# Performance work log

Hardware: AMD Instinct MI355X
Metric: run time of the kernel (lower is better)

Reference implementation:

```python
import math
import jax, jax.numpy as jnp
import numpy as np

D_MODEL = 1024
N_HEADS = 16
D_K = D_MODEL // N_HEADS
ROPE_BASE = 10000.0


def _rope_cos_sin(T, d, dtype=jnp.float32):
    inv_freq = 1.0 / (ROPE_BASE ** (jnp.arange(0, d, 2, dtype=jnp.float32) / d))
    ang = jnp.arange(T, dtype=jnp.float32)[:, None] * inv_freq[None, :]  # (T, d/2)
    emb = jnp.concatenate([ang, ang], axis=-1)  # (T, d)
    return jnp.cos(emb).astype(dtype), jnp.sin(emb).astype(dtype)


def _rotate_half(x):
    half = x.shape[-1] // 2
    return jnp.concatenate([-x[..., half:], x[..., :half]], axis=-1)


def _apply_rope(q, k):
    # q,k: (B, H, T, d_k)
    T = q.shape[2]
    cos, sin = _rope_cos_sin(T, q.shape[-1], q.dtype)  # (T, d_k)
    cos = cos[None, None]
    sin = sin[None, None]
    q = q * cos + _rotate_half(q) * sin
    k = k * cos + _rotate_half(k) * sin
    return q, k


def setup_inputs() -> dict:
    key = jax.random.key(0)
    ks = jax.random.split(key, 9)
    B, T = 4, 2048
    std = 1.0 / math.sqrt(D_MODEL)
    inp = {
        "x": jax.random.normal(ks[0], (B, T, D_MODEL), dtype=jnp.float32),
        "mask": jnp.zeros((B, 1, 1, T), dtype=bool),
        "Wq": jax.random.normal(ks[1], (D_MODEL, D_MODEL), jnp.float32) * std,
        "bq": jnp.zeros((D_MODEL,), jnp.float32),
        "Wk": jax.random.normal(ks[2], (D_MODEL, D_MODEL), jnp.float32) * std,
        "bk": jnp.zeros((D_MODEL,), jnp.float32),
        "Wv": jax.random.normal(ks[3], (D_MODEL, D_MODEL), jnp.float32) * std,
        "bv": jnp.zeros((D_MODEL,), jnp.float32),
        "Wo": jax.random.normal(ks[4], (D_MODEL, D_MODEL), jnp.float32) * std,
        "bo": jnp.zeros((D_MODEL,), jnp.float32),
    }
    return inp


def reference(x, mask, Wq, bq, Wk, bk, Wv, bv, Wo, bo):
    B, T, _ = x.shape
    H, dk = N_HEADS, D_K

    def proj(W, b):
        y = jnp.einsum("btd,ed->bte", x, W) + b  # nn.Linear: x @ W.T + b
        return y.reshape(B, T, H, dk).transpose(0, 2, 1, 3)  # (B,H,T,dk)

    q = proj(Wq, bq)
    k = proj(Wk, bk)
    v = proj(Wv, bv)
    q, k = _apply_rope(q, k)

    scale = math.sqrt(dk)
    scores = jnp.einsum("bhqd,bhkd->bhqk", q, k) / scale  # (B,H,T,T)
    neg = jnp.asarray(jnp.finfo(scores.dtype).min, scores.dtype)
    scores = jnp.where(mask, neg, scores)
    attn = jax.nn.softmax(scores, axis=-1)
    out = jnp.einsum("bhqk,bhkd->bhqd", attn, v)  # (B,H,T,dk)
    out = out.transpose(0, 2, 1, 3).reshape(B, T, H * dk)
    return jnp.einsum("btd,ed->bte", out, Wo) + bo
```

## Files before the change

### kernel.cpp

```cpp
#include <hip/hip_runtime.h>
#include <cstdint>

#define TSEQ   2048
#define NHEAD  16
#define DMODEL 1024
#define BSZ    4
#define MTOK   (BSZ*TSEQ)

typedef float  f32x4  __attribute__((ext_vector_type(4)));
typedef float  f32x16 __attribute__((ext_vector_type(16)));
typedef __bf16 bf16x8 __attribute__((ext_vector_type(8)));
typedef __bf16 bf16x4 __attribute__((ext_vector_type(4)));

static __device__ __forceinline__ f32x4 mfma16(bf16x8 a, bf16x8 b, f32x4 c) {
  return __builtin_amdgcn_mfma_f32_16x16x32_bf16(a, b, c, 0, 0, 0);
}
static __device__ __forceinline__ f32x16 mfma32(bf16x8 a, bf16x8 b, f32x16 c) {
  return __builtin_amdgcn_mfma_f32_32x32x16_bf16(a, b, c, 0, 0, 0);
}

#if __has_builtin(__builtin_amdgcn_exp2f)
#define EXP2(x) __builtin_amdgcn_exp2f(x)
#else
#define EXP2(x) exp2f(x)
#endif

static __device__ __forceinline__ uint32_t pk2(float lo, float hi) {
  union { __bf16 h[2]; uint32_t u; } cv;
  cv.h[0] = (__bf16)lo; cv.h[1] = (__bf16)hi;
  return cv.u;
}

static __device__ __forceinline__ void lds_cp16(void* lds, const void* g) {
  __builtin_amdgcn_global_load_lds(
      (__attribute__((address_space(1))) unsigned int*)(uintptr_t)g,
      (__attribute__((address_space(3))) unsigned int*)lds,
      16, 0, 0);
}


__global__ __launch_bounds__(256) void prep_cvt(
    const float* __restrict__ x,  const float* __restrict__ wq,
    const float* __restrict__ wk, const float* __restrict__ wv,
    const float* __restrict__ wo,
    __bf16* __restrict__ xb,  __bf16* __restrict__ wqb,
    __bf16* __restrict__ wkb, __bf16* __restrict__ wvb,
    __bf16* __restrict__ wob,
    float* __restrict__ ct, float* __restrict__ st)
{
  const int blk = blockIdx.x;
  if (blk >= 6144) {
    int i = (blk - 6144) * 256 + threadIdx.x;
    int t = i >> 5, d = i & 31;
    float inv = exp2f(-0.41524101186091903f * (float)d);
    float a = (float)t * inv;
    ct[i] = __cosf(a);
    st[i] = __sinf(a);
    return;
  }
  size_t i = (size_t)blk * 256 + threadIdx.x;
  const float* src; __bf16* dst; size_t base;
  if (i < 1048576) { src = x; dst = xb; base = i * 8; }
  else {
    size_t j = i - 1048576;
    int w = (int)(j >> 17);
    base = (j & 131071) * 8;
    switch (w) {
      case 0:  src = wq; dst = wqb; break;
      case 1:  src = wk; dst = wkb; break;
      case 2:  src = wv; dst = wvb; break;
      default: src = wo; dst = wob; break;
    }
  }
  float4 a = *reinterpret_cast<const float4*>(src + base);
  float4 b = *reinterpret_cast<const float4*>(src + base + 4);
  bf16x8 o;
  o[0] = (__bf16)a.x; o[1] = (__bf16)a.y; o[2] = (__bf16)a.z; o[3] = (__bf16)a.w;
  o[4] = (__bf16)b.x; o[5] = (__bf16)b.y; o[6] = (__bf16)b.z; o[7] = (__bf16)b.w;
  *reinterpret_cast<bf16x8*>(dst + base) = o;
}

__global__ __launch_bounds__(256) void gemm_qkv(
    const __bf16* __restrict__ A,
    const __bf16* __restrict__ Wqb, const __bf16* __restrict__ Wkb,
    const __bf16* __restrict__ Wvb,
    const float* __restrict__ bqp, const float* __restrict__ bkp,
    const float* __restrict__ bvp,
    __bf16* __restrict__ Qf, __bf16* __restrict__ Kf, __bf16* __restrict__ Vf,
    const float* __restrict__ ct, const float* __restrict__ st)
{
  __shared__ __align__(16) __bf16 As[128 * 32];
  __shared__ __align__(16) __bf16 Bs[128 * 32];

  const int bx = blockIdx.x;
  const int region = bx >> 3;
  const int n0 = (bx & 7) * 128;
  const __bf16* W = region == 0 ? Wqb : region == 1 ? Wkb : Wvb;
  const float* bias = region == 0 ? bqp : region == 1 ? bkp : bvp;
  const float qscale = region == 0 ? 0.18033688011112042f : 1.0f;

  const int tid  = threadIdx.x;
  const int wid  = tid >> 6, lane = tid & 63;
  const int wr   = wid >> 1, wc = wid & 1;
  const int lr   = lane & 15, lg = lane >> 4;
  const int m0   = blockIdx.y * 128;

  const int c0   = wid * 2;
  const int srow = lane >> 2;
  const int scol = (lane & 3) * 8;
  const __bf16* gA0 = A + (size_t)(m0 + c0 * 16 + srow) * 1024 + scol;
  const __bf16* gA1 = A + (size_t)(m0 + c0 * 16 + 16 + srow) * 1024 + scol;
  const __bf16* gB0 = W + (size_t)(n0 + c0 * 16 + srow) * 1024 + scol;
  const __bf16* gB1 = W + (size_t)(n0 + c0 * 16 + 16 + srow) * 1024 + scol;
  __bf16* lA0 = As + c0 * 512 + lane * 8;
  __bf16* lA1 = As + (c0 + 1) * 512 + lane * 8;
  __bf16* lB0 = Bs + c0 * 512 + lane * 8;
  __bf16* lB1 = Bs + (c0 + 1) * 512 + lane * 8;

  f32x4 acc[4][4] = {};

  for (int kt = 0; kt < 32; ++kt) {
    const int k0 = kt * 32;
    __syncthreads();
    lds_cp16(lA0, gA0 + k0);
    lds_cp16(lA1, gA1 + k0);
    lds_cp16(lB0, gB0 + k0);
    lds_cp16(lB1, gB1 + k0);
    __syncthreads();

    bf16x8 af[4], bf[4];
#pragma unroll
    for (int mi = 0; mi < 4; ++mi)
      af[mi] = *reinterpret_cast<const bf16x8*>(As + (wr * 64 + mi * 16 + lr) * 32 + lg * 8);
#pragma unroll
    for (int nj = 0; nj < 4; ++nj)
      bf[nj] = *reinterpret_cast<const bf16x8*>(Bs + (wc * 64 + nj * 16 + lr) * 32 + lg * 8);
#pragma unroll
    for (int mi = 0; mi < 4; ++mi)
#pragma unroll
      for (int nj = 0; nj < 4; ++nj)
        acc[mi][nj] = mfma16(af[mi], bf[nj], acc[mi][nj]);
  }

  float bcol[4];
#pragma unroll
  for (int nj = 0; nj < 4; ++nj) bcol[nj] = bias[n0 + wc * 64 + nj * 16 + lr];

  if (region < 2) {
    __bf16* Of = region == 0 ? Qf : Kf;
#pragma unroll
    for (int mi = 0; mi < 4; ++mi) {
      const int mbase = m0 + wr * 64 + mi * 16 + lg * 4;
#pragma unroll
      for (int r = 0; r < 4; ++r) {
        const int m = mbase + r;
        const int t = m & (TSEQ - 1);
        float v[4];
#pragma unroll
        for (int nj = 0; nj < 4; ++nj) v[nj] = acc[mi][nj][r] + bcol[nj];
#pragma unroll
        for (int nj = 0; nj < 4; ++nj) {
          const int idx = ((nj & 1) << 4) + lr;
          const float c = ct[t * 32 + idx];
          const float s = st[t * 32 + idx];
          const float rot = (nj < 2) ? -v[nj + 2] : v[nj - 2];
          const float o = (v[nj] * c + rot * s) * qscale;
          const int n = n0 + wc * 64 + nj * 16 + lr;
          const int d = n & 63, h = n >> 6;
          const int bh = ((m >> 11) << 4) + h;
          const size_t fidx =
              ((((size_t)bh * 64 + (t >> 5)) * 4 + (d >> 4)) * 2 + ((d >> 3) & 1)) * 256
              + (t & 31) * 8 + (d & 7);
          Of[fidx] = (__bf16)o;
        }
      }
    }
  } else {
#pragma unroll
    for (int mi = 0; mi < 4; ++mi) {
      const int mbase = m0 + wr * 64 + mi * 16 + lg * 4;
      const int bidx = mbase >> 11;
      const int tbase = mbase & (TSEQ - 1);
#pragma unroll
      for (int nj = 0; nj < 4; ++nj) {
        const int n = n0 + wc * 64 + nj * 16 + lr;
        const int h = n >> 6, d = n & 63;
        const int bh = bidx * 16 + h;
        bf16x4 pk;
#pragma unroll
        for (int r = 0; r < 4; ++r) pk[r] = (__bf16)(acc[mi][nj][r] + bcol[nj]);
        const size_t fidx =
            (((((size_t)bh * 32 + (tbase >> 6)) * 4 + ((tbase >> 4) & 3)) * 2
              + ((tbase >> 3) & 1)) * 2 + (d >> 5)) * 256
            + (d & 31) * 8 + (tbase & 7);
        *reinterpret_cast<bf16x4*>(Vf + fidx) = pk;
      }
    }
  }
}

__global__ __launch_bounds__(256) void gemm_out(
    const __bf16* __restrict__ A, const __bf16* __restrict__ W,
    const float* __restrict__ bias, float* __restrict__ Of)
{
  __shared__ __align__(16) __bf16 As[128 * 32];
  __shared__ __align__(16) __bf16 Bs[128 * 32];

  const int tid  = threadIdx.x;
  const int wid  = tid >> 6, lane = tid & 63;
  const int wr   = wid >> 1, wc = wid & 1;
  const int lr   = lane & 15, lg = lane >> 4;
  const int n0   = blockIdx.x * 128;
  const int m0   = blockIdx.y * 128;

  const int c0   = wid * 2;
  const int srow = lane >> 2;
  const int scol = (lane & 3) * 8;
  const __bf16* gA0 = A + (size_t)(m0 + c0 * 16 + srow) * 1024 + scol;
  const __bf16* gA1 = A + (size_t)(m0 + c0 * 16 + 16 + srow) * 1024 + scol;
  const __bf16* gB0 = W + (size_t)(n0 + c0 * 16 + srow) * 1024 + scol;
  const __bf16* gB1 = W + (size_t)(n0 + c0 * 16 + 16 + srow) * 1024 + scol;
  __bf16* lA0 = As + c0 * 512 + lane * 8;
  __bf16* lA1 = As + (c0 + 1) * 512 + lane * 8;
  __bf16* lB0 = Bs + c0 * 512 + lane * 8;
  __bf16* lB1 = Bs + (c0 + 1) * 512 + lane * 8;

  f32x4 acc[4][4] = {};

  for (int kt = 0; kt < 32; ++kt) {
    const int k0 = kt * 32;
    __syncthreads();
    lds_cp16(lA0, gA0 + k0);
    lds_cp16(lA1, gA1 + k0);
    lds_cp16(lB0, gB0 + k0);
    lds_cp16(lB1, gB1 + k0);
    __syncthreads();

    bf16x8 af[4], bf[4];
#pragma unroll
    for (int mi = 0; mi < 4; ++mi)
      af[mi] = *reinterpret_cast<const bf16x8*>(As + (wr * 64 + mi * 16 + lr) * 32 + lg * 8);
#pragma unroll
    for (int nj = 0; nj < 4; ++nj)
      bf[nj] = *reinterpret_cast<const bf16x8*>(Bs + (wc * 64 + nj * 16 + lr) * 32 + lg * 8);
#pragma unroll
    for (int mi = 0; mi < 4; ++mi)
#pragma unroll
      for (int nj = 0; nj < 4; ++nj)
        acc[mi][nj] = mfma16(af[mi], bf[nj], acc[mi][nj]);
  }

  float bcol[4];
#pragma unroll
  for (int nj = 0; nj < 4; ++nj) bcol[nj] = bias[n0 + wc * 64 + nj * 16 + lr];

#pragma unroll
  for (int mi = 0; mi < 4; ++mi) {
    const int mbase = m0 + wr * 64 + mi * 16 + lg * 4;
#pragma unroll
    for (int r = 0; r < 4; ++r) {
      const int m = mbase + r;
#pragma unroll
      for (int nj = 0; nj < 4; ++nj) {
        const int n = n0 + wc * 64 + nj * 16 + lr;
        Of[(size_t)m * 1024 + n] = acc[mi][nj][r] + bcol[nj];
      }
    }
  }
}

__global__ __launch_bounds__(128, 3) void attn_k(
    const __bf16* __restrict__ QKq, const __bf16* __restrict__ QKk,
    const __bf16* __restrict__ Vf, __bf16* __restrict__ O)
{
  const int tid = threadIdx.x, wid = tid >> 6, lane = tid & 63;
  const int ql = lane & 31, hl = lane >> 5;
  const int bid = blockIdx.x;
  const int bh = (bid & 7) * 8 + (bid >> 8);
  const int qt = (bid >> 3) & 31;
  const int b = bh >> 4, h = bh & 15;
  const int qbase = qt * 64 + wid * 32;
  const size_t tokQ = (size_t)b * TSEQ + qbase;
  const int laneoff = hl * 256 + ql * 8;

  const __bf16* Qb = QKq + ((size_t)bh * 64 + (qbase >> 5)) * 2048;
  bf16x8 qf[4];
#pragma unroll
  for (int ch = 0; ch < 4; ++ch)
    qf[ch] = *reinterpret_cast<const bf16x8*>(Qb + ch * 512 + laneoff);

  bf16x8 ones8;
#pragma unroll
  for (int j = 0; j < 8; ++j) ones8[j] = (__bf16)1.0f;

  f32x16 ot[2] = {};
  f32x16 lsum = {};

  const __bf16* Kbh = QKk + (size_t)bh * 64 * 2048;
  const __bf16* Vbh = Vf + (size_t)bh * 32 * 4096;

  for (int kv = 0; kv < TSEQ; kv += 64) {
    const __bf16* Vb = Vbh + (size_t)(kv >> 6) * 4096;
    bf16x8 va[2][4];
#pragma unroll
    for (int db = 0; db < 2; ++db)
#pragma unroll
      for (int c = 0; c < 4; ++c)
        va[db][c] = *reinterpret_cast<const bf16x8*>(
            Vb + c * 1024 + hl * 512 + db * 256 + ql * 8);

    bf16x8 ka[2][4];
#pragma unroll
    for (int s = 0; s < 2; ++s) {
      const __bf16* Kb = Kbh + (size_t)((kv >> 5) + s) * 2048;
#pragma unroll
      for (int ch = 0; ch < 4; ++ch)
        ka[s][ch] = *reinterpret_cast<const bf16x8*>(Kb + ch * 512 + laneoff);
    }

    f32x16 sx[2] = {};
    __builtin_amdgcn_s_setprio(1);
#pragma unroll
    for (int s = 0; s < 2; ++s)
#pragma unroll
      for (int ch = 0; ch < 4; ++ch)
        sx[s] = mfma32(ka[s][ch], qf[ch], sx[s]);
    __builtin_amdgcn_s_setprio(0);

    uint32_t pd[2][4][2];
#pragma unroll
    for (int s = 0; s < 2; ++s)
#pragma unroll
      for (int g = 0; g < 4; ++g)
#pragma unroll
        for (int hf = 0; hf < 2; ++hf)
          pd[s][g][hf] = pk2(EXP2(sx[s][4 * g + 2 * hf]),
                             EXP2(sx[s][4 * g + 2 * hf + 1]));

    uint32_t kp[2][2][2], rv[2][2][2];
#pragma unroll
    for (int s = 0; s < 2; ++s)
#pragma unroll
      for (int cc = 0; cc < 2; ++cc)
#pragma unroll
        for (int hf = 0; hf < 2; ++hf) {
          const uint32_t sendv = hl ? pd[s][2 * cc][hf] : pd[s][2 * cc + 1][hf];
          rv[s][cc][hf] = __shfl_xor(sendv, 32, 64);
          kp[s][cc][hf] = hl ? pd[s][2 * cc + 1][hf] : pd[s][2 * cc][hf];
        }

#pragma unroll
    for (int c = 0; c < 4; ++c) {
      const int s = c >> 1, cc = c & 1;
      union { uint32_t u[4]; bf16x8 v; } fb;
      fb.u[0] = hl ? rv[s][cc][0] : kp[s][cc][0];
      fb.u[1] = hl ? rv[s][cc][1] : kp[s][cc][1];
      fb.u[2] = hl ? kp[s][cc][0] : rv[s][cc][0];
      fb.u[3] = hl ? kp[s][cc][1] : rv[s][cc][1];
      __builtin_amdgcn_s_setprio(1);
      ot[0] = mfma32(va[0][c], fb.v, ot[0]);
      ot[1] = mfma32(va[1][c], fb.v, ot[1]);
      lsum  = mfma32(ones8,    fb.v, lsum);
      __builtin_amdgcn_s_setprio(0);
    }
  }

  const float inv = 1.0f / lsum[0];
  __bf16* Orow = O + (tokQ + ql) * 1024 + h * 64;
#pragma unroll
  for (int db = 0; db < 2; ++db)
#pragma unroll
    for (int g = 0; g < 4; ++g) {
      bf16x4 ov;
#pragma unroll
      for (int r = 0; r < 4; ++r) ov[r] = (__bf16)(ot[db][4 * g + r] * inv);
      *reinterpret_cast<bf16x4*>(Orow + db * 32 + 8 * g + 4 * hl) = ov;
    }
}

extern "C" void kernel_launch(void* const* d_in, const int* in_sizes, int n_in,
                              void* d_out, int out_size, void* d_ws, size_t ws_size,
                              hipStream_t stream) {
  (void)in_sizes; (void)n_in; (void)out_size; (void)ws_size;
  const float* x  = (const float*)d_in[0];
  const float* Wq = (const float*)d_in[2];
  const float* bq = (const float*)d_in[3];
  const float* Wk = (const float*)d_in[4];
  const float* bk = (const float*)d_in[5];
  const float* Wv = (const float*)d_in[6];
  const float* bvp= (const float*)d_in[7];
  const float* Wo = (const float*)d_in[8];
  const float* bo = (const float*)d_in[9];
  float* out = (float*)d_out;

  char* ws = (char*)d_ws;
  size_t off = 0;
  auto carve = [&](size_t bytes) { void* p = ws + off; off += (bytes + 255) & ~(size_t)255; return p; };
  __bf16* xb  = (__bf16*)carve((size_t)MTOK * DMODEL * 2);
  __bf16* qb  = (__bf16*)carve((size_t)MTOK * DMODEL * 2);
  __bf16* kb_ = (__bf16*)carve((size_t)MTOK * DMODEL * 2);
  __bf16* vt  = (__bf16*)carve((size_t)MTOK * DMODEL * 2);
  __bf16* ab  = (__bf16*)carve((size_t)MTOK * DMODEL * 2);
  __bf16* wqb = (__bf16*)carve((size_t)DMODEL * DMODEL * 2);
  __bf16* wkb = (__bf16*)carve((size_t)DMODEL * DMODEL * 2);
  __bf16* wvb = (__bf16*)carve((size_t)DMODEL * DMODEL * 2);
  __bf16* wob = (__bf16*)carve((size_t)DMODEL * DMODEL * 2);
  float*  ct  = (float*)carve((size_t)TSEQ * 32 * 4);
  float*  st  = (float*)carve((size_t)TSEQ * 32 * 4);

  prep_cvt<<<6400, 256, 0, stream>>>(x, Wq, Wk, Wv, Wo, xb, wqb, wkb, wvb, wob, ct, st);

  gemm_qkv<<<dim3(24, 64), 256, 0, stream>>>(xb, wqb, wkb, wvb, bq, bk, bvp,
                                             qb, kb_, vt, ct, st);

  attn_k<<<2048, 128, 0, stream>>>(qb, kb_, vt, ab);

  gemm_out<<<dim3(8, 64), 256, 0, stream>>>(ab, wob, bo, out);
}
```

Baseline: 227.2 us.

## Software-pipeline attention loop over 32-key tiles and drop ones-MFMA row sum

Restructures the attention inner loop to work on 32-key tiles. The next K tile is prefetched and the PV MFMAs of the previous tile are interleaved with the QK MFMAs and exp of the current tile, so loads and softmax overlap with matrix work. The row-sum MFMA against a ones vector is replaced by a scalar fp32 sum of the exponentials plus a cross-half shuffle at the end. This cuts MFMA count by a third but adds VALU adds, and the sum now uses unrounded fp32 values instead of bf16, which slightly changes numerics.

```diff
diff --git a/kernel.cpp b/kernel.cpp
--- a/kernel.cpp
+++ b/kernel.cpp
@@ -282,6 +282,7 @@
   const int qbase = qt * 64 + wid * 32;
   const size_t tokQ = (size_t)b * TSEQ + qbase;
   const int laneoff = hl * 256 + ql * 8;
+  const int vlaneoff = hl * 512 + ql * 8;
 
   const __bf16* Qb = QKq + ((size_t)bh * 64 + (qbase >> 5)) * 2048;
   bf16x8 qf[4];
@@ -289,93 +290,101 @@
   for (int ch = 0; ch < 4; ++ch)
     qf[ch] = *reinterpret_cast<const bf16x8*>(Qb + ch * 512 + laneoff);
 
-  bf16x8 ones8;
-#pragma unroll
-  for (int j = 0; j < 8; ++j) ones8[j] = (__bf16)1.0f;
-
-  f32x16 ot[2] = {};
-  f32x16 lsum = {};
-
   const __bf16* Kbh = QKk + (size_t)bh * 64 * 2048;
   const __bf16* Vbh = Vf + (size_t)bh * 32 * 4096;
 
-  for (int kv = 0; kv < TSEQ; kv += 64) {
-    const __bf16* Vb = Vbh + (size_t)(kv >> 6) * 4096;
-    bf16x8 va[2][4];
-#pragma unroll
-    for (int db = 0; db < 2; ++db)
-#pragma unroll
-      for (int c = 0; c < 4; ++c)
-        va[db][c] = *reinterpret_cast<const bf16x8*>(
-            Vb + c * 1024 + hl * 512 + db * 256 + ql * 8);
-
-    bf16x8 ka[2][4];
-#pragma unroll
-    for (int s = 0; s < 2; ++s) {
-      const __bf16* Kb = Kbh + (size_t)((kv >> 5) + s) * 2048;
-#pragma unroll
-      for (int ch = 0; ch < 4; ++ch)
-        ka[s][ch] = *reinterpret_cast<const bf16x8*>(Kb + ch * 512 + laneoff);
+  f32x16 ot0 = {}, ot1 = {};
+  float l_run = 0.0f;
+
+  bf16x8 ka[4];
+  bf16x8 va[4];
+  union FB { uint32_t u[4]; bf16x8 v; } fb0, fb1;
+  f32x16 sx;
+
+#define LOADK(t) {                                                     \
+    const __bf16* Kb_ = Kbh + (size_t)(t) * 2048;                      \
+    _Pragma("unroll")                                                  \
+    for (int ch = 0; ch < 4; ++ch)                                     \
+      ka[ch] = *reinterpret_cast<const bf16x8*>(Kb_ + ch * 512 + laneoff); }
+
+#define LOADV(t) {                                                     \
+    const __bf16* Vb_ = Vbh + (size_t)((t) >> 1) * 4096 + ((t) & 1) * 2048; \
+    _Pragma("unroll")                                                  \
+    for (int db = 0; db < 2; ++db)                                     \
+      _Pragma("unroll")                                                \
+      for (int cc = 0; cc < 2; ++cc)                                   \
+        va[db * 2 + cc] = *reinterpret_cast<const bf16x8*>(            \
+            Vb_ + cc * 1024 + db * 256 + vlaneoff); }
+
+#define QKSTEP {                                                       \
+    sx = (f32x16){};                                                   \
+    __builtin_amdgcn_s_setprio(1);                                     \
+    _Pragma("unroll")                                                  \
+    for (int ch = 0; ch < 4; ++ch) sx = mfma32(ka[ch], qf[ch], sx);    \
+    __builtin_amdgcn_s_setprio(0); }
+
+#define PVSTEP {                                                       \
+    __builtin_amdgcn_s_setprio(1);                                     \
+    ot0 = mfma32(va[0], fb0.v, ot0);                                   \
+    ot1 = mfma32(va[2], fb0.v, ot1);                                   \
+    ot0 = mfma32(va[1], fb1.v, ot0);                                   \
+    ot1 = mfma32(va[3], fb1.v, ot1);                                   \
+    __builtin_amdgcn_s_setprio(0); }
+
+#define SMSTEP {                                                       \
+    float p[16];                                                       \
+    _Pragma("unroll")                                                  \
+    for (int i_ = 0; i_ < 16; ++i_) p[i_] = EXP2(sx[i_]);              \
+    l_run += (((p[0]+p[1])+(p[2]+p[3]))+((p[4]+p[5])+(p[6]+p[7])))     \
+           + (((p[8]+p[9])+(p[10]+p[11]))+((p[12]+p[13])+(p[14]+p[15]))); \
+    uint32_t pd[4][2];                                                 \
+    _Pragma("unroll")                                                  \
+    for (int g = 0; g < 4; ++g)                                        \
+      _Pragma("unroll")                                                \
+      for (int hf = 0; hf < 2; ++hf)                                   \
+        pd[g][hf] = pk2(p[4*g + 2*hf], p[4*g + 2*hf + 1]);             \
+    _Pragma("unroll")                                                  \
+    for (int c_ = 0; c_ < 2; ++c_) {                                   \
+      _Pragma("unroll")                                                \
+      for (int hf = 0; hf < 2; ++hf) {                                 \
+        const uint32_t sendv = hl ? pd[2*c_][hf] : pd[2*c_+1][hf];     \
+        const uint32_t rv = __shfl_xor(sendv, 32, 64);                 \
+        const uint32_t kp = hl ? pd[2*c_+1][hf] : pd[2*c_][hf];        \
+        FB& f_ = c_ ? fb1 : fb0;                                       \
+        f_.u[hf]     = hl ? rv : kp;                                   \
+        f_.u[2 + hf] = hl ? kp : rv;                                   \
+      }                                                                \
+    } }
+
+  LOADK(0);
+  QKSTEP;
+  LOADK(1);
+  LOADV(0);
+  SMSTEP;
+
+  for (int i = 1; i < 64; ++i) {
+    QKSTEP;
+    LOADK(i + 1);
+    PVSTEP;
+    LOADV(i);
+    SMSTEP;
+  }
+  PVSTEP;
+
+  const float l = l_run + __shfl_xor(l_run, 32, 64);
+  const float inv = 1.0f / l;
+  __bf16* Orow = O + (tokQ + ql) * 1024 + h * 64;
+#pragma unroll
+  for (int g = 0; g < 4; ++g) {
+    bf16x4 ov0, ov1;
+#pragma unroll
+    for (int r = 0; r < 4; ++r) {
+      ov0[r] = (__bf16)(ot0[4 * g + r] * inv);
+      ov1[r] = (__bf16)(ot1[4 * g + r] * inv);
     }
-
-    f32x16 sx[2] = {};
-    __builtin_amdgcn_s_setprio(1);
-#pragma unroll
-    for (int s = 0; s < 2; ++s)
-#pragma unroll
-      for (int ch = 0; ch < 4; ++ch)
-        sx[s] = mfma32(ka[s][ch], qf[ch], sx[s]);
-    __builtin_amdgcn_s_setprio(0);
-
-    uint32_t pd[2][4][2];
-#pragma unroll
-    for (int s = 0; s < 2; ++s)
-#pragma unroll
-      for (int g = 0; g < 4; ++g)
-#pragma unroll
-        for (int hf = 0; hf < 2; ++hf)
-          pd[s][g][hf] = pk2(EXP2(sx[s][4 * g + 2 * hf]),
-                             EXP2(sx[s][4 * g + 2 * hf + 1]));
-
-    uint32_t kp[2][2][2], rv[2][2][2];
-#pragma unroll
-    for (int s = 0; s < 2; ++s)
-#pragma unroll
-      for (int cc = 0; cc < 2; ++cc)
-#pragma unroll
-        for (int hf = 0; hf < 2; ++hf) {
-          const uint32_t sendv = hl ? pd[s][2 * cc][hf] : pd[s][2 * cc + 1][hf];
-          rv[s][cc][hf] = __shfl_xor(sendv, 32, 64);
-          kp[s][cc][hf] = hl ? pd[s][2 * cc + 1][hf] : pd[s][2 * cc][hf];
-        }
-
-#pragma unroll
-    for (int c = 0; c < 4; ++c) {
-      const int s = c >> 1, cc = c & 1;
-      union { uint32_t u[4]; bf16x8 v; } fb;
-      fb.u[0] = hl ? rv[s][cc][0] : kp[s][cc][0];
-      fb.u[1] = hl ? rv[s][cc][1] : kp[s][cc][1];
-      fb.u[2] = hl ? kp[s][cc][0] : rv[s][cc][0];
-      fb.u[3] = hl ? kp[s][cc][1] : rv[s][cc][1];
-      __builtin_amdgcn_s_setprio(1);
-      ot[0] = mfma32(va[0][c], fb.v, ot[0]);
-      ot[1] = mfma32(va[1][c], fb.v, ot[1]);
-      lsum  = mfma32(ones8,    fb.v, lsum);
-      __builtin_amdgcn_s_setprio(0);
-    }
-  }
-
-  const float inv = 1.0f / lsum[0];
-  __bf16* Orow = O + (tokQ + ql) * 1024 + h * 64;
-#pragma unroll
-  for (int db = 0; db < 2; ++db)
-#pragma unroll
-    for (int g = 0; g < 4; ++g) {
-      bf16x4 ov;
-#pragma unroll
-      for (int r = 0; r < 4; ++r) ov[r] = (__bf16)(ot[db][4 * g + r] * inv);
-      *reinterpret_cast<bf16x4*>(Orow + db * 32 + 8 * g + 4 * hl) = ov;
-    }
+    *reinterpret_cast<bf16x4*>(Orow + 8 * g + 4 * hl) = ov0;
+    *reinterpret_cast<bf16x4*>(Orow + 32 + 8 * g + 4 * hl) = ov1;
+  }
 }
 
 extern "C" void kernel_launch(void* const* d_in, const int* in_sizes, int n_in,
```

Measured after the change: 219.7 us. 3.3% less time.

## Stage K/V tiles through double-buffered LDS shared by four waves in attention

Applied to the files above, without the earlier changes.

The attention kernel now uses 256-thread blocks covering 128 queries. Each KV tile of 32 keys is copied once into a double-buffered shared-memory buffer with async LDS copies and read by all four waves, replacing per-wave global loads. The row-sum is now accumulated with scalar adds instead of an extra MFMA against a ones vector. This cuts redundant global/L2 traffic and MFMA work, at the cost of a block-wide barrier every tile and a smaller KV step per iteration. It relies on lds_cp16 being defined in the hidden part of the file.

```diff
diff --git a/kernel.cpp b/kernel.cpp
--- a/kernel.cpp
+++ b/kernel.cpp
@@ -269,113 +269,115 @@
   }
 }
 
-__global__ __launch_bounds__(128, 3) void attn_k(
+__global__ __launch_bounds__(256, 4) void attn_k(
     const __bf16* __restrict__ QKq, const __bf16* __restrict__ QKk,
     const __bf16* __restrict__ Vf, __bf16* __restrict__ O)
 {
+  __shared__ __align__(16) char Kv[2][8192];
+
   const int tid = threadIdx.x, wid = tid >> 6, lane = tid & 63;
   const int ql = lane & 31, hl = lane >> 5;
   const int bid = blockIdx.x;
-  const int bh = (bid & 7) * 8 + (bid >> 8);
-  const int qt = (bid >> 3) & 31;
+  const int bh = (bid & 7) * 8 + (bid >> 7);
+  const int qt = (bid >> 3) & 15;
   const int b = bh >> 4, h = bh & 15;
-  const int qbase = qt * 64 + wid * 32;
+  const int qbase = qt * 128 + wid * 32;
   const size_t tokQ = (size_t)b * TSEQ + qbase;
-  const int laneoff = hl * 256 + ql * 8;
 
   const __bf16* Qb = QKq + ((size_t)bh * 64 + (qbase >> 5)) * 2048;
   bf16x8 qf[4];
 #pragma unroll
   for (int ch = 0; ch < 4; ++ch)
-    qf[ch] = *reinterpret_cast<const bf16x8*>(Qb + ch * 512 + laneoff);
-
-  bf16x8 ones8;
-#pragma unroll
-  for (int j = 0; j < 8; ++j) ones8[j] = (__bf16)1.0f;
-
-  f32x16 ot[2] = {};
-  f32x16 lsum = {};
-
-  const __bf16* Kbh = QKk + (size_t)bh * 64 * 2048;
-  const __bf16* Vbh = Vf + (size_t)bh * 32 * 4096;
-
-  for (int kv = 0; kv < TSEQ; kv += 64) {
-    const __bf16* Vb = Vbh + (size_t)(kv >> 6) * 4096;
-    bf16x8 va[2][4];
+    qf[ch] = *reinterpret_cast<const bf16x8*>(Qb + ch * 512 + hl * 256 + ql * 8);
+
+  const char* Ksrc = (const char*)QKk + (size_t)bh * 262144;
+  const char* Vsrc = (const char*)Vf + (size_t)bh * 262144;
+  const int soff = wid * 1024 + lane * 16;
+
+  f32x16 ot0 = {}, ot1 = {};
+  float l_run = 0.0f;
+
+#define STAGE(t, bi) {                                   \
+    lds_cp16(Kv[bi] + soff,        Ksrc + (size_t)(t) * 4096 + soff); \
+    lds_cp16(Kv[bi] + 4096 + soff, Vsrc + (size_t)(t) * 4096 + soff); }
+
+  STAGE(0, 0);
+  __syncthreads();
+
+  for (int i = 0; i < 64; ++i) {
+    const int cur = i & 1;
+    const char* buf = Kv[cur];
+    if (i < 63) STAGE(i + 1, cur ^ 1);
+
+    bf16x8 ka[4];
+#pragma unroll
+    for (int ch = 0; ch < 4; ++ch)
+      ka[ch] = *reinterpret_cast<const bf16x8*>(buf + ch * 1024 + lane * 16);
+    f32x16 sx = {};
+    __builtin_amdgcn_s_setprio(1);
+#pragma unroll
+    for (int ch = 0; ch < 4; ++ch) sx = mfma32(ka[ch], qf[ch], sx);
+    __builtin_amdgcn_s_setprio(0);
+
+    bf16x8 va[4];
 #pragma unroll
     for (int db = 0; db < 2; ++db)
 #pragma unroll
-      for (int c = 0; c < 4; ++c)
-        va[db][c] = *reinterpret_cast<const bf16x8*>(
-            Vb + c * 1024 + hl * 512 + db * 256 + ql * 8);
-
-    bf16x8 ka[2][4];
-#pragma unroll
-    for (int s = 0; s < 2; ++s) {
-      const __bf16* Kb = Kbh + (size_t)((kv >> 5) + s) * 2048;
-#pragma unroll
-      for (int ch = 0; ch < 4; ++ch)
-        ka[s][ch] = *reinterpret_cast<const bf16x8*>(Kb + ch * 512 + laneoff);
-    }
-
-    f32x16 sx[2] = {};
+      for (int cc = 0; cc < 2; ++cc)
+        va[db * 2 + cc] = *reinterpret_cast<const bf16x8*>(
+            buf + 4096 + cc * 2048 + hl * 1024 + db * 512 + ql * 16);
+
+    float p[16];
+#pragma unroll
+    for (int i_ = 0; i_ < 16; ++i_) p[i_] = EXP2(sx[i_]);
+    l_run += (((p[0]+p[1])+(p[2]+p[3]))+((p[4]+p[5])+(p[6]+p[7])))
+           + (((p[8]+p[9])+(p[10]+p[11]))+((p[12]+p[13])+(p[14]+p[15])));
+    uint32_t pd[4][2];
+#pragma unroll
+    for (int g = 0; g < 4; ++g)
+#pragma unroll
+      for (int hf = 0; hf < 2; ++hf)
+        pd[g][hf] = pk2(p[4 * g + 2 * hf], p[4 * g + 2 * hf + 1]);
+
+    union FB { uint32_t u[4]; bf16x8 v; } fb0, fb1;
+#pragma unroll
+    for (int cc = 0; cc < 2; ++cc) {
+      FB& f = cc ? fb1 : fb0;
+#pragma unroll
+      for (int hf = 0; hf < 2; ++hf) {
+        const uint32_t sendv = hl ? pd[2 * cc][hf] : pd[2 * cc + 1][hf];
+        const uint32_t rv = __shfl_xor(sendv, 32, 64);
+        const uint32_t kp = hl ? pd[2 * cc + 1][hf] : pd[2 * cc][hf];
+        f.u[hf]     = hl ? rv : kp;
+        f.u[2 + hf] = hl ? kp : rv;
+      }
+    }
+
     __builtin_amdgcn_s_setprio(1);
-#pragma unroll
-    for (int s = 0; s < 2; ++s)
-#pragma unroll
-      for (int ch = 0; ch < 4; ++ch)
-        sx[s] = mfma32(ka[s][ch], qf[ch], sx[s]);
+    ot0 = mfma32(va[0], fb0.v, ot0);
+    ot1 = mfma32(va[2], fb0.v, ot1);
+    ot0 = mfma32(va[1], fb1.v, ot0);
+    ot1 = mfma32(va[3], fb1.v, ot1);
     __builtin_amdgcn_s_setprio(0);
 
-    uint32_t pd[2][4][2];
-#pragma unroll
-    for (int s = 0; s < 2; ++s)
-#pragma unroll
-      for (int g = 0; g < 4; ++g)
-#pragma unroll
-        for (int hf = 0; hf < 2; ++hf)
-          pd[s][g][hf] = pk2(EXP2(sx[s][4 * g + 2 * hf]),
-                             EXP2(sx[s][4 * g + 2 * hf + 1]));
-
-    uint32_t kp[2][2][2], rv[2][2][2];
-#pragma unroll
-    for (int s = 0; s < 2; ++s)
-#pragma unroll
-      for (int cc = 0; cc < 2; ++cc)
-#pragma unroll
-        for (int hf = 0; hf < 2; ++hf) {
-          const uint32_t sendv = hl ? pd[s][2 * cc][hf] : pd[s][2 * cc + 1][hf];
-          rv[s][cc][hf] = __shfl_xor(sendv, 32, 64);
-          kp[s][cc][hf] = hl ? pd[s][2 * cc + 1][hf] : pd[s][2 * cc][hf];
-        }
-
-#pragma unroll
-    for (int c = 0; c < 4; ++c) {
-      const int s = c >> 1, cc = c & 1;
-      union { uint32_t u[4]; bf16x8 v; } fb;
-      fb.u[0] = hl ? rv[s][cc][0] : kp[s][cc][0];
-      fb.u[1] = hl ? rv[s][cc][1] : kp[s][cc][1];
-      fb.u[2] = hl ? kp[s][cc][0] : rv[s][cc][0];
-      fb.u[3] = hl ? kp[s][cc][1] : rv[s][cc][1];
-      __builtin_amdgcn_s_setprio(1);
-      ot[0] = mfma32(va[0][c], fb.v, ot[0]);
-      ot[1] = mfma32(va[1][c], fb.v, ot[1]);
-      lsum  = mfma32(ones8,    fb.v, lsum);
-      __builtin_amdgcn_s_setprio(0);
-    }
-  }
-
-  const float inv = 1.0f / lsum[0];
+    __syncthreads();
+  }
+#undef STAGE
+
+  const float l = l_run + __shfl_xor(l_run, 32, 64);
+  const float inv = 1.0f / l;
   __bf16* Orow = O + (tokQ + ql) * 1024 + h * 64;
 #pragma unroll
-  for (int db = 0; db < 2; ++db)
-#pragma unroll
-    for (int g = 0; g < 4; ++g) {
-      bf16x4 ov;
-#pragma unroll
-      for (int r = 0; r < 4; ++r) ov[r] = (__bf16)(ot[db][4 * g + r] * inv);
-      *reinterpret_cast<bf16x4*>(Orow + db * 32 + 8 * g + 4 * hl) = ov;
-    }
+  for (int g = 0; g < 4; ++g) {
+    bf16x4 ov0, ov1;
+#pragma unroll
+    for (int r = 0; r < 4; ++r) {
+      ov0[r] = (__bf16)(ot0[4 * g + r] * inv);
+      ov1[r] = (__bf16)(ot1[4 * g + r] * inv);
+    }
+    *reinterpret_cast<bf16x4*>(Orow + 8 * g + 4 * hl) = ov0;
+    *reinterpret_cast<bf16x4*>(Orow + 32 + 8 * g + 4 * hl) = ov1;
+  }
 }
 
 extern "C" void kernel_launch(void* const* d_in, const int* in_sizes, int n_in,
@@ -413,7 +415,7 @@
   gemm_qkv<<<dim3(24, 64), 256, 0, stream>>>(xb, wqb, wkb, wvb, bq, bk, bvp,
                                              qb, kb_, vt, ct, st);
 
-  attn_k<<<2048, 128, 0, stream>>>(qb, kb_, vt, ab);
+  attn_k<<<1024, 256, 0, stream>>>(qb, kb_, vt, ab);
 
   gemm_out<<<dim3(8, 64), 256, 0, stream>>>(ab, wob, bo, out);
 }
```

New measurement: 209.8 us. -7.6%, faster.
